# Optimization experiments

Measured on AMD Instinct MI355X. Metric: run time of the kernel, lower is better.

Reference implementation:

```python
import jax, jax.numpy as jnp
import numpy as np

N_CAM, N_REF, N_HEADS, EMBD = 6, 4, 8, 256
OUT = 10
L = OUT * OUT            # seq_len = output_size^2
HS = EMBD // N_HEADS
BS = 2


def setup_inputs() -> dict:
    key = jax.random.key(0)
    k1, k2, k3 = jax.random.split(key, 3)
    # C'*H'*W' must equal seq_len*embd = 100*256 = 25600 -> (256,10,10)
    single_frame_feature = jax.random.normal(k1, (BS, 1, N_CAM, 256, 10, 10), jnp.float32)
    bev_query = jax.random.normal(k2, (BS, L, EMBD), jnp.float32)
    W_v = jax.random.normal(k3, (N_CAM * EMBD, N_REF * EMBD), jnp.float32) / np.float32(np.sqrt(N_CAM * EMBD))
    b_v = jnp.zeros((N_REF * EMBD,), jnp.float32)
    return {"single_frame_feature": single_frame_feature, "bev_query": bev_query, "W_v": W_v, "b_v": b_v}


def reference(single_frame_feature, bev_query, W_v, b_v):
    bs, _, n_cam, C, H, W = single_frame_feature.shape
    _, seq_len, embd = bev_query.shape
    nh, hs, n_ref = N_HEADS, embd // N_HEADS, N_REF
    R = n_cam * n_ref  # repeat factor

    # (bs, n_cam, seq_len, embd) -- C*H*W == seq_len*embd by construction
    feat = single_frame_feature.reshape(bs, n_cam, seq_len, embd)

    # q: (bs, seq_len, nh, hs) repeated over cameras x ref points -> (bs, R*L, nh, hs)
    q = bev_query.reshape(bs, seq_len, nh, hs)
    q = jnp.tile(q, (1, R, 1, 1))

    # k: camera features broadcast over ref points, ordered (cam, ref, L)
    k = feat.reshape(bs, n_cam, 1, seq_len, nh, hs)
    k = jnp.broadcast_to(k, (bs, n_cam, n_ref, seq_len, nh, hs)).reshape(bs, R * seq_len, nh, hs)

    # v: per-location linear mixing cameras into n_ref value slots (self.v)
    v_in = feat.transpose(0, 2, 1, 3).reshape(bs, seq_len, n_cam * embd)
    v = v_in @ W_v + b_v                                   # (bs, L, n_ref*embd)
    v = v.reshape(bs, seq_len, n_ref, nh, hs).transpose(0, 2, 1, 3, 4)  # (bs, n_ref, L, nh, hs)
    v = jnp.broadcast_to(v[:, None], (bs, n_cam, n_ref, seq_len, nh, hs)).reshape(bs, R * seq_len, nh, hs)

    # scaled dot-product attention (dropout is identity at eval)
    scores = jnp.einsum('bqhd,bkhd->bhqk', q, k) / jnp.sqrt(jnp.float32(hs))
    att = jax.nn.softmax(scores, axis=-1)                  # (bs, nh, R*L, R*L)
    out = jnp.einsum('bhqk,bkhd->bqhd', att, v)            # (bs, R*L, nh, hs)

    # fold the R repeated views back to the BEV grid (uniform ref weights)
    out = out.reshape(bs, R, seq_len, embd).mean(axis=1)   # (bs, L, embd)
    return out
```

## Files before the change

kernel.cpp:

```cpp
#include <hip/hip_runtime.h>

#define N_CAM   6
#define N_HEADS 8
#define EMBD    256
#define HS      32
#define L       100
#define BS      2
#define CAM_STRIDE (L * EMBD)
#define CK      (N_CAM * L)

#define WS_WSUM 0
#define WS_KTR  (WS_WSUM + 1536 * 256)
#define WS_P    (WS_KTR + 2 * N_HEADS * 8 * CK * 4)
#define WS_E    (WS_P + 200 * 256 * 4)

__global__ __launch_bounds__(256) void prep_kernel(const float* __restrict__ feat,
                                                   const float4* __restrict__ Wv4,
                                                   float* __restrict__ ws) {
    const int t = threadIdx.x;
    if (blockIdx.x < 96) {
        __shared__ float tile[100 * 33];
        int blk = blockIdx.x;
        int b   = blk / 48;
        int rem = blk - b * 48;
        int cam = rem >> 3;
        int h   = rem & 7;
        const float4* src4 = reinterpret_cast<const float4*>(
            feat + (size_t)(b * N_CAM + cam) * CAM_STRIDE + h * HS);
        for (int idx = t; idx < 100 * 8; idx += 256) {
            int sk = idx >> 3;
            int d4 = idx & 7;
            float4 v = src4[sk * (EMBD / 4) + d4];
            float* dst = &tile[sk * 33 + d4 * 4];
            dst[0] = v.x; dst[1] = v.y; dst[2] = v.z; dst[3] = v.w;
        }
        __syncthreads();
        float4* ktr4 = reinterpret_cast<float4*>(ws + WS_KTR)
                     + (size_t)(b * N_HEADS + h) * 8 * CK + cam * L;
        for (int idx = t; idx < 8 * 100; idx += 256) {
            int d4 = idx / 100;
            int sk = idx - d4 * 100;
            const float* s = &tile[sk * 33 + d4 * 4];
            ktr4[(size_t)d4 * CK + sk] = make_float4(s[0], s[1], s[2], s[3]);
        }
    } else {
        int tid = (blockIdx.x - 96) * 256 + t;
        int i  = tid >> 6;
        int e4 = tid & 63;
        const float4* row = Wv4 + (size_t)i * 256;
        float4 a = row[e4];
        float4 b = row[64 + e4];
        float4 c = row[128 + e4];
        float4 d = row[192 + e4];
        float4 o;
        o.x = a.x + b.x + c.x + d.x;
        o.y = a.y + b.y + c.y + d.y;
        o.z = a.z + b.z + c.z + d.z;
        o.w = a.w + b.w + c.w + d.w;
        ((float4*)(ws + WS_WSUM))[(size_t)i * 64 + e4] = o;
    }
}

__global__ __launch_bounds__(256) void mid_kernel(const float* __restrict__ feat,
                                                  const float* __restrict__ query,
                                                  const float* __restrict__ ws_r,
                                                  float* __restrict__ ws_w) {
    const int t = threadIdx.x;
    if (blockIdx.x < 200) {
        __shared__ float a_tile[4 * 384];
        const int rg = blockIdx.x >> 2;
        const int c  = blockIdx.x & 3;
        const int r0 = rg * 4;
        const int k0 = c * 384;

        for (int i = t; i < 4 * 384; i += 256) {
            int j  = i / 384;
            int kk = i - j * 384;
            int k  = k0 + kk;
            int cam = k >> 8, e2 = k & 255;
            int row = r0 + j;
            int b = row >= 100;
            int s = row - b * 100;
            a_tile[i] = feat[(size_t)(b * N_CAM + cam) * CAM_STRIDE + s * EMBD + e2];
        }
        __syncthreads();

        float acc0 = 0.f, acc1 = 0.f, acc2 = 0.f, acc3 = 0.f;
        const float* wp = ws_r + WS_WSUM + (size_t)k0 * 256 + t;
#pragma unroll 32
        for (int kk = 0; kk < 384; ++kk) {
            float w = wp[(size_t)kk * 256];
            acc0 += a_tile[kk] * w;
            acc1 += a_tile[384 + kk] * w;
            acc2 += a_tile[768 + kk] * w;
            acc3 += a_tile[1152 + kk] * w;
        }

        float* P = ws_w + WS_P;
        P[((size_t)(r0 + 0) * 256 + t) * 4 + c] = acc0;
        P[((size_t)(r0 + 1) * 256 + t) * 4 + c] = acc1;
        P[((size_t)(r0 + 2) * 256 + t) * 4 + c] = acc2;
        P[((size_t)(r0 + 3) * 256 + t) * 4 + c] = acc3;
    } else {
        __shared__ float q_s[4 * 32];
        __shared__ float es[4 * CK];
        int idx = blockIdx.x - 200;
        int b   = idx / 200;
        int rem = idx - b * 200;
        int h   = rem / 25;
        int sqt = rem - h * 25;
        int sq0 = sqt * 4;

        if (t < 128)
            q_s[t] = query[(size_t)(b * L + sq0 + (t >> 5)) * EMBD + h * HS + (t & 31)];
        __syncthreads();

        const float scale = 0.17677669529663687f;
        const float4* kt4 = reinterpret_cast<const float4*>(ws_r + WS_KTR)
                          + (size_t)(b * N_HEADS + h) * 8 * CK;

#pragma unroll
        for (int i = 0; i < 3; ++i) {
            int ck = t + i * 256;
            if (ck < CK) {
                float acc0 = 0.f, acc1 = 0.f, acc2 = 0.f, acc3 = 0.f;
#pragma unroll
                for (int d4 = 0; d4 < 8; ++d4) {
                    float4 kv = kt4[(size_t)d4 * CK + ck];
                    const float* q0 = &q_s[0 * 32 + d4 * 4];
                    const float* q1 = &q_s[1 * 32 + d4 * 4];
                    const float* q2 = &q_s[2 * 32 + d4 * 4];
                    const float* q3 = &q_s[3 * 32 + d4 * 4];
                    acc0 += q0[0] * kv.x + q0[1] * kv.y + q0[2] * kv.z + q0[3] * kv.w;
                    acc1 += q1[0] * kv.x + q1[1] * kv.y + q1[2] * kv.z + q1[3] * kv.w;
                    acc2 += q2[0] * kv.x + q2[1] * kv.y + q2[2] * kv.z + q2[3] * kv.w;
                    acc3 += q3[0] * kv.x + q3[1] * kv.y + q3[2] * kv.z + q3[3] * kv.w;
                }
                es[0 * CK + ck] = __expf(acc0 * scale);
                es[1 * CK + ck] = __expf(acc1 * scale);
                es[2 * CK + ck] = __expf(acc2 * scale);
                es[3 * CK + ck] = __expf(acc3 * scale);
            }
        }
        __syncthreads();

        float* E = ws_w + WS_E;
        for (int p = t; p < 4 * L; p += 256) {
            int sj = p / 100, sk = p - sj * 100;
            float e = 0.f;
#pragma unroll
            for (int cam = 0; cam < N_CAM; ++cam)
                e += es[sj * CK + cam * L + sk];
            E[((size_t)(b * L + sq0 + sj) * N_HEADS + h) * L + sk] = e;
        }
    }
}

__global__ __launch_bounds__(256) void out_kernel(const float* __restrict__ ws,
                                                  const float* __restrict__ b_v,
                                                  float* __restrict__ out) {
    __shared__ float E_s[2 * N_HEADS * L];
    const int t   = threadIdx.x;
    const int b   = blockIdx.x / 50;
    const int sq0 = (blockIdx.x - b * 50) * 2;

    const float* E = ws + WS_E + (size_t)(b * L + sq0) * N_HEADS * L;
    for (int i = t; i < 2 * N_HEADS * L; i += 256) E_s[i] = E[i];
    __syncthreads();

    const int h = t >> 5;
    float sumE0 = 0.f, sumE1 = 0.f;
#pragma unroll 4
    for (int sk = 0; sk < L; ++sk) {
        sumE0 += E_s[h * L + sk];
        sumE1 += E_s[N_HEADS * L + h * L + sk];
    }

    float bias = b_v[t] + b_v[256 + t] + b_v[512 + t] + b_v[768 + t];

    const float4* p4 = (const float4*)(ws + WS_P) + (size_t)b * L * 256 + t;
    float acc0 = 0.f, acc1 = 0.f;
#pragma unroll 16
    for (int sk = 0; sk < L; ++sk) {
        float4 p = p4[(size_t)sk * 256];
        float s = p.x + p.y + p.z + p.w;
        acc0 += E_s[h * L + sk] * s;
        acc1 += E_s[N_HEADS * L + h * L + sk] * s;
    }

    out[(size_t)(b * L + sq0 + 0) * EMBD + t] = (acc0 + sumE0 * bias) * (0.25f / sumE0);
    out[(size_t)(b * L + sq0 + 1) * EMBD + t] = (acc1 + sumE1 * bias) * (0.25f / sumE1);
}

extern "C" void kernel_launch(void* const* d_in, const int* in_sizes, int n_in,
                              void* d_out, int out_size, void* d_ws, size_t ws_size,
                              hipStream_t stream) {
    const float* feat  = (const float*)d_in[0];
    const float* query = (const float*)d_in[1];
    const float4* Wv   = (const float4*)d_in[2];
    const float* bv    = (const float*)d_in[3];
    float* outp = (float*)d_out;
    float* ws   = (float*)d_ws;

    prep_kernel<<<480, 256, 0, stream>>>(feat, Wv, ws);
    mid_kernel<<<600, 256, 0, stream>>>(feat, query, ws, ws);
    out_kernel<<<100, 256, 0, stream>>>(ws, bv, outp);
}
```

Before: 98.74 us.

## Fuse three stage kernels into one cooperative persistent kernel with grid syncs

Merges the prep, mid and out kernels into a single cooperative launch of 256 blocks that runs the three stages as job loops separated by grid-wide syncs. Stages two and three hand out jobs dynamically through atomic counters kept in the workspace. The aim is to drop two kernel launch gaps and their tail effects. In exchange it pays for grid-sync barriers and serial atomic job fetching, and it has fewer blocks than the original grids, so each block does more jobs.

```diff
diff --git a/kernel.cpp b/kernel.cpp
--- a/kernel.cpp
+++ b/kernel.cpp
@@ -1,4 +1,7 @@
 #include <hip/hip_runtime.h>
+#include <hip/hip_cooperative_groups.h>
+
+namespace cg = cooperative_groups;
 
 #define N_CAM   6
 #define N_HEADS 8
@@ -13,6 +16,217 @@
 #define WS_KTR  (WS_WSUM + 1536 * 256)
 #define WS_P    (WS_KTR + 2 * N_HEADS * 8 * CK * 4)
 #define WS_E    (WS_P + 200 * 256 * 4)
+#define WS_CNT  (WS_E + 200 * N_HEADS * L)
+
+#define S1_JOBS 480
+#define S2_JOBS 600
+#define S3_JOBS 100
+
+__global__ __launch_bounds__(256) void fused_kernel(const float* __restrict__ feat,
+                                                    const float* __restrict__ query,
+                                                    const float4* __restrict__ Wv4,
+                                                    const float* __restrict__ b_v,
+                                                    float* __restrict__ out,
+                                                    float* __restrict__ ws) {
+    cg::grid_group grid = cg::this_grid();
+    __shared__ float smem[3400];
+    __shared__ unsigned job_s;
+    const int t = threadIdx.x;
+
+    unsigned* cnt2 = (unsigned*)(ws + WS_CNT);
+    unsigned* cnt3 = cnt2 + 1;
+
+    if (blockIdx.x == 0 && t == 0) {
+        atomicExch(cnt2, 0u);
+        atomicExch(cnt3, 0u);
+    }
+
+    for (int job = blockIdx.x; job < S1_JOBS; job += gridDim.x) {
+        __syncthreads();
+        if (job < 96) {
+            float* tile = smem;
+            int b   = job / 48;
+            int rem = job - b * 48;
+            int cam = rem >> 3;
+            int h   = rem & 7;
+            const float4* src4 = reinterpret_cast<const float4*>(
+                feat + (size_t)(b * N_CAM + cam) * CAM_STRIDE + h * HS);
+            for (int idx = t; idx < 100 * 8; idx += 256) {
+                int sk = idx >> 3;
+                int d4 = idx & 7;
+                float4 v = src4[sk * (EMBD / 4) + d4];
+                float* dst = &tile[sk * 33 + d4 * 4];
+                dst[0] = v.x; dst[1] = v.y; dst[2] = v.z; dst[3] = v.w;
+            }
+            __syncthreads();
+            float4* ktr4 = reinterpret_cast<float4*>(ws + WS_KTR)
+                         + (size_t)(b * N_HEADS + h) * 8 * CK + cam * L;
+            for (int idx = t; idx < 8 * 100; idx += 256) {
+                int d4 = idx / 100;
+                int sk = idx - d4 * 100;
+                const float* s = &tile[sk * 33 + d4 * 4];
+                ktr4[(size_t)d4 * CK + sk] = make_float4(s[0], s[1], s[2], s[3]);
+            }
+        } else {
+            int tid = (job - 96) * 256 + t;
+            int i  = tid >> 6;
+            int e4 = tid & 63;
+            const float4* row = Wv4 + (size_t)i * 256;
+            float4 a = row[e4];
+            float4 b = row[64 + e4];
+            float4 c = row[128 + e4];
+            float4 d = row[192 + e4];
+            float4 o;
+            o.x = a.x + b.x + c.x + d.x;
+            o.y = a.y + b.y + c.y + d.y;
+            o.z = a.z + b.z + c.z + d.z;
+            o.w = a.w + b.w + c.w + d.w;
+            ((float4*)(ws + WS_WSUM))[(size_t)i * 64 + e4] = o;
+        }
+    }
+
+    __threadfence();
+    grid.sync();
+
+    while (true) {
+        __syncthreads();
+        if (t == 0) job_s = atomicAdd(cnt2, 1u);
+        __syncthreads();
+        unsigned job = job_s;
+        if (job >= S2_JOBS) break;
+
+        if (job < 200) {
+            float* a_tile = smem;
+            const int rg = job >> 2;
+            const int c  = job & 3;
+            const int r0 = rg * 4;
+            const int k0 = c * 384;
+
+            for (int i = t; i < 4 * 384; i += 256) {
+                int j  = i / 384;
+                int kk = i - j * 384;
+                int k  = k0 + kk;
+                int cam = k >> 8, e2 = k & 255;
+                int row = r0 + j;
+                int b = row >= 100;
+                int s = row - b * 100;
+                a_tile[i] = feat[(size_t)(b * N_CAM + cam) * CAM_STRIDE + s * EMBD + e2];
+            }
+            __syncthreads();
+
+            float acc0 = 0.f, acc1 = 0.f, acc2 = 0.f, acc3 = 0.f;
+            const float* wp = ws + WS_WSUM + (size_t)k0 * 256 + t;
+#pragma unroll 32
+            for (int kk = 0; kk < 384; ++kk) {
+                float w = wp[(size_t)kk * 256];
+                acc0 += a_tile[kk] * w;
+                acc1 += a_tile[384 + kk] * w;
+                acc2 += a_tile[768 + kk] * w;
+                acc3 += a_tile[1152 + kk] * w;
+            }
+
+            float* P = ws + WS_P;
+            P[((size_t)(r0 + 0) * 256 + t) * 4 + c] = acc0;
+            P[((size_t)(r0 + 1) * 256 + t) * 4 + c] = acc1;
+            P[((size_t)(r0 + 2) * 256 + t) * 4 + c] = acc2;
+            P[((size_t)(r0 + 3) * 256 + t) * 4 + c] = acc3;
+        } else {
+            float* q_s = smem;
+            float* es  = smem + 128;
+            int idx = job - 200;
+            int b   = idx / 200;
+            int rem = idx - b * 200;
+            int h   = rem / 25;
+            int sqt = rem - h * 25;
+            int sq0 = sqt * 4;
+
+            if (t < 128)
+                q_s[t] = query[(size_t)(b * L + sq0 + (t >> 5)) * EMBD + h * HS + (t & 31)];
+            __syncthreads();
+
+            const float scale = 0.17677669529663687f;
+            const float4* kt4 = reinterpret_cast<const float4*>(ws + WS_KTR)
+                              + (size_t)(b * N_HEADS + h) * 8 * CK;
+
+#pragma unroll
+            for (int i = 0; i < 3; ++i) {
+                int ck = t + i * 256;
+                if (ck < CK) {
+                    float acc0 = 0.f, acc1 = 0.f, acc2 = 0.f, acc3 = 0.f;
+#pragma unroll
+                    for (int d4 = 0; d4 < 8; ++d4) {
+                        float4 kv = kt4[(size_t)d4 * CK + ck];
+                        const float* q0 = &q_s[0 * 32 + d4 * 4];
+                        const float* q1 = &q_s[1 * 32 + d4 * 4];
+                        const float* q2 = &q_s[2 * 32 + d4 * 4];
+                        const float* q3 = &q_s[3 * 32 + d4 * 4];
+                        acc0 += q0[0] * kv.x + q0[1] * kv.y + q0[2] * kv.z + q0[3] * kv.w;
+                        acc1 += q1[0] * kv.x + q1[1] * kv.y + q1[2] * kv.z + q1[3] * kv.w;
+                        acc2 += q2[0] * kv.x + q2[1] * kv.y + q2[2] * kv.z + q2[3] * kv.w;
+                        acc3 += q3[0] * kv.x + q3[1] * kv.y + q3[2] * kv.z + q3[3] * kv.w;
+                    }
+                    es[0 * CK + ck] = __expf(acc0 * scale);
+                    es[1 * CK + ck] = __expf(acc1 * scale);
+                    es[2 * CK + ck] = __expf(acc2 * scale);
+                    es[3 * CK + ck] = __expf(acc3 * scale);
+                }
+            }
+            __syncthreads();
+
+            float* E = ws + WS_E;
+            for (int p = t; p < 4 * L; p += 256) {
+                int sj = p / 100, sk = p - sj * 100;
+                float e = 0.f;
+#pragma unroll
+                for (int cam = 0; cam < N_CAM; ++cam)
+                    e += es[sj * CK + cam * L + sk];
+                E[((size_t)(b * L + sq0 + sj) * N_HEADS + h) * L + sk] = e;
+            }
+        }
+    }
+
+    __threadfence();
+    grid.sync();
+
+    while (true) {
+        __syncthreads();
+        if (t == 0) job_s = atomicAdd(cnt3, 1u);
+        __syncthreads();
+        unsigned job = job_s;
+        if (job >= S3_JOBS) break;
+
+        float* E_s = smem;
+        const int b   = job / 50;
+        const int sq0 = (job - b * 50) * 2;
+
+        const float* E = ws + WS_E + (size_t)(b * L + sq0) * N_HEADS * L;
+        for (int i = t; i < 2 * N_HEADS * L; i += 256) E_s[i] = E[i];
+        __syncthreads();
+
+        const int h = t >> 5;
+        float sumE0 = 0.f, sumE1 = 0.f;
+#pragma unroll 4
+        for (int sk = 0; sk < L; ++sk) {
+            sumE0 += E_s[h * L + sk];
+            sumE1 += E_s[N_HEADS * L + h * L + sk];
+        }
+
+        float bias = b_v[t] + b_v[256 + t] + b_v[512 + t] + b_v[768 + t];
+
+        const float4* p4 = (const float4*)(ws + WS_P) + (size_t)b * L * 256 + t;
+        float acc0 = 0.f, acc1 = 0.f;
+#pragma unroll 16
+        for (int sk = 0; sk < L; ++sk) {
+            float4 p = p4[(size_t)sk * 256];
+            float s = p.x + p.y + p.z + p.w;
+            acc0 += E_s[h * L + sk] * s;
+            acc1 += E_s[N_HEADS * L + h * L + sk] * s;
+        }
+
+        out[(size_t)(b * L + sq0 + 0) * EMBD + t] = (acc0 + sumE0 * bias) * (0.25f / sumE0);
+        out[(size_t)(b * L + sq0 + 1) * EMBD + t] = (acc1 + sumE1 * bias) * (0.25f / sumE1);
+    }
+}
 
 __global__ __launch_bounds__(256) void prep_kernel(const float* __restrict__ feat,
                                                    const float4* __restrict__ Wv4,
@@ -202,7 +416,14 @@
     float* outp = (float*)d_out;
     float* ws   = (float*)d_ws;
 
-    prep_kernel<<<480, 256, 0, stream>>>(feat, Wv, ws);
-    mid_kernel<<<600, 256, 0, stream>>>(feat, query, ws, ws);
-    out_kernel<<<100, 256, 0, stream>>>(ws, bv, outp);
+    void* args[] = {(void*)&feat, (void*)&query, (void*)&Wv, (void*)&bv,
+                    (void*)&outp, (void*)&ws};
+    hipError_t err = hipLaunchCooperativeKernel((const void*)fused_kernel,
+                                                dim3(256), dim3(256),
+                                                args, 0, stream);
+    if (err != hipSuccess) {
+        prep_kernel<<<480, 256, 0, stream>>>(feat, Wv, ws);
+        mid_kernel<<<600, 256, 0, stream>>>(feat, query, ws, ws);
+        out_kernel<<<100, 256, 0, stream>>>(ws, bv, outp);
+    }
 }
```

Result: slower. 232.3 us (+135.2%).
